# Performance work log

Measured on AMD Instinct MI355X. Metric: run time of the kernel, lower is better.

Reference implementation:

```python
import jax, jax.numpy as jnp
import numpy as np

HEADS = 8
DIM_HEAD = 64
DIM_COOR = 3
SCALE = (DIM_COOR * DIM_HEAD) ** -0.5


def setup_inputs() -> dict:
    key = jax.random.key(0)
    k1, k2, k3 = jax.random.split(key, 3)
    x = jax.random.normal(k1, (2, 2048, 256, 3), dtype=jnp.float32)
    w_qkv = jax.random.normal(k2, (1536, 256), dtype=jnp.float32)
    w_out = jax.random.normal(k3, (256, 512), dtype=jnp.float32)
    return {"x": x, "w_qkv": w_qkv, "w_out": w_out}


def reference(x, w_qkv, w_out):
    b, n, _, c = x.shape
    # VNLinear: contract feature dim, keep coord dim  -> [b, n, 3*h*d, c]
    qkv = jnp.einsum('bnic,oi->bnoc', x, w_qkv)
    q, k, v = jnp.split(qkv, 3, axis=-2)  # each [b, n, h*d, c]

    def to_heads(t):
        return t.reshape(b, n, HEADS, DIM_HEAD, c).transpose(0, 2, 1, 3, 4)  # b h n d c

    q, k, v = map(to_heads, (q, k, v))
    q = q * SCALE
    # scores sum over head-dim AND coordinate-dim
    sim = jnp.einsum('bhidc,bhjdc->bhij', q, k)
    attn = jax.nn.softmax(sim, axis=-1)
    out = jnp.einsum('bhij,bhjdc->bhidc', attn, v)  # coord dim preserved
    out = out.transpose(0, 2, 1, 3, 4).reshape(b, n, HEADS * DIM_HEAD, c)
    return jnp.einsum('bnic,oi->bnoc', out, w_out)
```

## Files before the change

### kernel.cpp

```cpp
#include <hip/hip_runtime.h>
#include <hip/hip_bf16.h>

#define SCALE 0.07216878364870322f
#define LOG2E 1.4426950408889634f

typedef __bf16 bf16x8 __attribute__((ext_vector_type(8)));
typedef float f32x16 __attribute__((ext_vector_type(16)));
typedef float f32x4v __attribute__((ext_vector_type(4)));
typedef unsigned int u32x4 __attribute__((ext_vector_type(4)));
typedef unsigned int u32x2 __attribute__((ext_vector_type(2)));
typedef unsigned short u16;

#define MFMA(a, b, c) __builtin_amdgcn_mfma_f32_32x32x16_bf16(a, b, c, 0, 0, 0)
#define MFMA16(a, b, c) __builtin_amdgcn_mfma_f32_16x16x32_bf16(a, b, c, 0, 0, 0)

__device__ __forceinline__ u16 b16(float v) { return __builtin_bit_cast(u16, (__bf16)v); }
__device__ __forceinline__ float fb16(u16 u) {
    unsigned int t = (unsigned int)u << 16;
    return __builtin_bit_cast(float, t);
}
__device__ __forceinline__ unsigned int splitpack(float v) {
    u16 h = b16(v);
    float r = v - fb16(h);
    return (unsigned int)h | ((unsigned int)b16(r) << 16);
}
__device__ __forceinline__ unsigned int pack2(float a, float b) {
    return (unsigned int)b16(a) | ((unsigned int)b16(b) << 16);
}
__device__ __forceinline__ void gload16(const void* g, void* l) {
    __builtin_amdgcn_global_load_lds((const __attribute__((address_space(1))) void*)g,
                                     (__attribute__((address_space(3))) void*)l, 16, 0, 0);
}

__global__ __launch_bounds__(256) void qkv_mfma(const float* __restrict__ x,
                                                const float* __restrict__ wq,
                                                u16* __restrict__ Qhi, u16* __restrict__ Qlo,
                                                u16* __restrict__ KVf) {
    __shared__ unsigned int ldsr[2][32][196];
    const int tid = threadIdx.x;
    const int lane = tid & 63, w = tid >> 6, hf = lane >> 5, l31 = lane & 31;
    const int lq = lane & 15, gq = lane >> 4;
    const int id = blockIdx.x;
    const int xcd = id & 7;
    const int jj = id >> 3;
    const int nb = xcd * 4 + jj / 24;
    const int ot = jj % 24;
    const int o0 = ot * 64;
    const int b = nb >> 4;
    const int n0 = (nb & 15) * 128;
    const int nw0 = n0 + w * 32;
    const int part = o0 >> 9;
    const int h = (o0 >> 6) & 7;
    const int bh = b * 8 + h;

    const float* xp = x + ((size_t)(b * 2048 + nw0 + l31)) * 768 + hf * 24;
    const float* wp0 = wq + (size_t)(o0 + l31) * 256 + hf * 8;
    const float* wp1 = wp0 + 32 * 256;

    f32x16 acc[3][2] = {};
    #pragma unroll 2
    for (int k0 = 0; k0 < 16; ++k0) {
        float xf[24], wf0[8], wf1[8];
        #pragma unroll
        for (int q = 0; q < 6; ++q) {
            f32x4v t = *(const f32x4v*)(xp + k0 * 48 + q * 4);
            xf[q * 4 + 0] = t[0]; xf[q * 4 + 1] = t[1];
            xf[q * 4 + 2] = t[2]; xf[q * 4 + 3] = t[3];
        }
        {
            f32x4v t0 = *(const f32x4v*)(wp0 + k0 * 16);
            f32x4v t1 = *(const f32x4v*)(wp0 + k0 * 16 + 4);
            f32x4v t2 = *(const f32x4v*)(wp1 + k0 * 16);
            f32x4v t3 = *(const f32x4v*)(wp1 + k0 * 16 + 4);
            #pragma unroll
            for (int e = 0; e < 4; ++e) {
                wf0[e] = t0[e]; wf0[4 + e] = t1[e];
                wf1[e] = t2[e]; wf1[4 + e] = t3[e];
            }
        }
        bf16x8 xh[3], xl[3], wh[2], wl[2];
        #pragma unroll
        for (int c = 0; c < 3; ++c)
            #pragma unroll
            for (int e = 0; e < 8; ++e) {
                float v = xf[e * 3 + c];
                __bf16 hi = (__bf16)v;
                xh[c][e] = hi;
                xl[c][e] = (__bf16)(v - (float)hi);
            }
        #pragma unroll
        for (int e = 0; e < 8; ++e) {
            { float v = wf0[e]; __bf16 hi = (__bf16)v; wh[0][e] = hi; wl[0][e] = (__bf16)(v - (float)hi); }
            { float v = wf1[e]; __bf16 hi = (__bf16)v; wh[1][e] = hi; wl[1][e] = (__bf16)(v - (float)hi); }
        }
        #pragma unroll
        for (int c = 0; c < 3; ++c)
            #pragma unroll
            for (int ot2 = 0; ot2 < 2; ++ot2) {
                acc[c][ot2] = MFMA(xh[c], wh[ot2], acc[c][ot2]);
                acc[c][ot2] = MFMA(xl[c], wh[ot2], acc[c][ot2]);
                acc[c][ot2] = MFMA(xh[c], wl[ot2], acc[c][ot2]);
            }
    }

    #pragma unroll
    for (int round = 0; round < 2; ++round) {
        __syncthreads();
        if ((w >> 1) == round) {
            unsigned int (*L)[196] = ldsr[w & 1];
            #pragma unroll
            for (int c = 0; c < 3; ++c)
                #pragma unroll
                for (int ot2 = 0; ot2 < 2; ++ot2)
                    #pragma unroll
                    for (int r = 0; r < 16; ++r) {
                        float v = acc[c][ot2][r];
                        if (part == 0) v *= (SCALE * LOG2E);
                        int nn = (r & 3) + 8 * (r >> 2) + 4 * hf;
                        int dcol = 3 * (ot2 * 32 + l31) + c;
                        L[nn][dcol] = (part == 2) ? (unsigned int)b16(v) : splitpack(v);
                    }
            if (part < 2) {
                #pragma unroll
                for (int is = 0; is < 2; ++is)
                    #pragma unroll
                    for (int kc = 0; kc < 6; ++kc) {
                        const unsigned int* p = &L[is * 16 + lq][kc * 32 + gq * 8];
                        u32x4 a = *(const u32x4*)p;
                        u32x4 bq = *(const u32x4*)(p + 4);
                        u32x4 hi = { (a[0] & 0xffffu) | (a[1] << 16), (a[2] & 0xffffu) | (a[3] << 16),
                                     (bq[0] & 0xffffu) | (bq[1] << 16), (bq[2] & 0xffffu) | (bq[3] << 16) };
                        u32x4 lo = { (a[0] >> 16) | (a[1] & 0xffff0000u), (a[2] >> 16) | (a[3] & 0xffff0000u),
                                     (bq[0] >> 16) | (bq[1] & 0xffff0000u), (bq[2] >> 16) | (bq[3] & 0xffff0000u) };
                        if (part == 0) {
                            size_t off = ((size_t)(bh * 128 + (nw0 >> 4) + is) * 6 + kc) * 512 + lane * 8;
                            *(u32x4*)(Qhi + off) = hi;
                            *(u32x4*)(Qlo + off) = lo;
                        } else {
                            size_t off = (size_t)(bh * 64 + (nw0 >> 5)) * 18432 + (is * 6 + kc) * 512 + lane * 8;
                            *(u32x4*)(KVf + off) = hi;
                            *(u32x4*)(KVf + off + 6144) = lo;
                        }
                    }
            } else {
                u16* vp = KVf + (size_t)(bh * 64 + (nw0 >> 5)) * 18432 + 12288 + lane * 8;
                #pragma unroll
                for (int d = 0; d < 12; ++d) {
                    unsigned int t[8];
                    #pragma unroll
                    for (int e = 0; e < 8; ++e)
                        t[e] = L[gq * 8 + e][d * 16 + lq];
                    u32x4 pk = { (t[0] & 0xffffu) | (t[1] << 16), (t[2] & 0xffffu) | (t[3] << 16),
                                 (t[4] & 0xffffu) | (t[5] << 16), (t[6] & 0xffffu) | (t[7] << 16) };
                    *(u32x4*)(vp + d * 512) = pk;
                }
            }
        }
    }
}

__global__ __launch_bounds__(256, 2) void attn_mfma(
    const u16* __restrict__ Qhi, const u16* __restrict__ Qlo,
    const u16* __restrict__ KVf, u16* __restrict__ OpA, u16* __restrict__ OpB,
    float2* __restrict__ MLp) {
    __shared__ __align__(16) u16 lds[2][18432];
    const int tid = threadIdx.x;
    const int lane = tid & 63;
    const int wl = tid >> 6;
    const int g = lane >> 4;
    const int i = lane & 15;
    const int id = blockIdx.x;
    const int rem = id >> 3;
    const int grp = ((rem >> 4) << 3) | (id & 7);
    const int itile = rem & 15;
    const int bh = grp >> 1;
    const int half = grp & 1;

    bf16x8 qh[2][6], ql[2][6];
    #pragma unroll
    for (int is = 0; is < 2; ++is) {
        size_t qb = (size_t)(bh * 128 + itile * 8 + wl * 2 + is) * 3072 + (size_t)lane * 8;
        #pragma unroll
        for (int kc = 0; kc < 6; ++kc) {
            qh[is][kc] = *(const bf16x8*)(Qhi + qb + kc * 512);
            ql[is][kc] = *(const bf16x8*)(Qlo + qb + kc * 512);
        }
    }

    const char* gKV = (const char*)KVf + (size_t)bh * 2359296;
    auto stage = [&](int buf, int jtAbs) {
        const char* src = gKV + (size_t)jtAbs * 36864;
        char* dst = (char*)&lds[buf][0];
        #pragma unroll
        for (int s = 0; s < 9; ++s) {
            const int c16 = (tid + s * 256) * 16;
            gload16(src + c16, dst + c16);
        }
    };

    const int jt0 = half * 32;
    stage(0, jt0);
    __syncthreads();
    int cur = 0;

    f32x4v o[2][12] = {};
    float m_run[2] = {-1e30f, -1e30f}, l_run[2] = {0.f, 0.f};

    for (int t = 0; t < 32; ++t) {
        if (t + 1 < 32) stage(cur ^ 1, jt0 + t + 1);
        const u16* L = &lds[cur][0];

        f32x4v s4[2][2] = {};
        __builtin_amdgcn_s_setprio(1);
        #pragma unroll
        for (int kc = 0; kc < 6; ++kc) {
            bf16x8 kh0 = *(const bf16x8*)&L[(unsigned)(kc * 512) + lane * 8];
            bf16x8 kh1 = *(const bf16x8*)&L[(unsigned)((6 + kc) * 512) + lane * 8];
            bf16x8 kl0 = *(const bf16x8*)&L[6144u + (unsigned)(kc * 512) + lane * 8];
            bf16x8 kl1 = *(const bf16x8*)&L[6144u + (unsigned)((6 + kc) * 512) + lane * 8];
            s4[0][0] = MFMA16(kh0, qh[0][kc], s4[0][0]);
            s4[0][1] = MFMA16(kh1, qh[0][kc], s4[0][1]);
            s4[1][0] = MFMA16(kh0, qh[1][kc], s4[1][0]);
            s4[1][1] = MFMA16(kh1, qh[1][kc], s4[1][1]);
            s4[0][0] = MFMA16(kh0, ql[0][kc], s4[0][0]);
            s4[0][1] = MFMA16(kh1, ql[0][kc], s4[0][1]);
            s4[1][0] = MFMA16(kh0, ql[1][kc], s4[1][0]);
            s4[1][1] = MFMA16(kh1, ql[1][kc], s4[1][1]);
            s4[0][0] = MFMA16(kl0, qh[0][kc], s4[0][0]);
            s4[0][1] = MFMA16(kl1, qh[0][kc], s4[0][1]);
            s4[1][0] = MFMA16(kl0, qh[1][kc], s4[1][0]);
            s4[1][1] = MFMA16(kl1, qh[1][kc], s4[1][1]);
        }
        __builtin_amdgcn_s_setprio(0);

        bf16x8 pb[2];
        #pragma unroll
        for (int is = 0; is < 2; ++is) {
            float pm = -1e30f;
            #pragma unroll
            for (int js = 0; js < 2; ++js)
                #pragma unroll
                for (int r = 0; r < 4; ++r) pm = fmaxf(pm, s4[is][js][r]);
            pm = fmaxf(pm, __shfl_xor(pm, 16, 64));
            pm = fmaxf(pm, __shfl_xor(pm, 32, 64));
            if (!__all(pm <= m_run[is] + 8.0f)) {
                float mnew = fmaxf(m_run[is], pm);
                float sc = exp2f(m_run[is] - mnew);
                l_run[is] *= sc;
                #pragma unroll
                for (int d = 0; d < 12; ++d) o[is][d] = o[is][d] * sc;
                m_run[is] = mnew;
            }
            float rs = 0.f;
            unsigned int w0[2], w1[2];
            #pragma unroll
            for (int js = 0; js < 2; ++js) {
                float p0 = exp2f(s4[is][js][0] - m_run[is]), p1 = exp2f(s4[is][js][1] - m_run[is]);
                float p2 = exp2f(s4[is][js][2] - m_run[is]), p3 = exp2f(s4[is][js][3] - m_run[is]);
                rs += (p0 + p1) + (p2 + p3);
                w0[js] = pack2(p0, p1);
                w1[js] = pack2(p2, p3);
            }
            rs += __shfl_xor(rs, 16, 64);
            rs += __shfl_xor(rs, 32, 64);
            l_run[is] += rs;

            u32x4 F;
            const int slA = ((g & 1) << 5) + i;
            const int slB = slA + 16;
            const bool ghi = (g >> 1) != 0;
            { unsigned a0 = __shfl((int)w0[0], slA, 64), a1 = __shfl((int)w0[1], slA, 64); F[0] = ghi ? a1 : a0; }
            { unsigned a0 = __shfl((int)w1[0], slA, 64), a1 = __shfl((int)w1[1], slA, 64); F[1] = ghi ? a1 : a0; }
            { unsigned a0 = __shfl((int)w0[0], slB, 64), a1 = __shfl((int)w0[1], slB, 64); F[2] = ghi ? a1 : a0; }
            { unsigned a0 = __shfl((int)w1[0], slB, 64), a1 = __shfl((int)w1[1], slB, 64); F[3] = ghi ? a1 : a0; }
            pb[is] = __builtin_bit_cast(bf16x8, F);
        }

        __builtin_amdgcn_s_setprio(1);
        #pragma unroll
        for (int d = 0; d < 12; ++d) {
            bf16x8 vf = *(const bf16x8*)&L[12288u + (unsigned)(d * 512) + lane * 8];
            o[0][d] = MFMA16(vf, pb[0], o[0][d]);
            o[1][d] = MFMA16(vf, pb[1], o[1][d]);
        }
        __builtin_amdgcn_s_setprio(0);

        if (t + 1 < 32) {
            __syncthreads();
            cur ^= 1;
        }
    }

    __syncthreads();
    u16* LS = &lds[0][0];
    #pragma unroll
    for (int is = 0; is < 2; ++is) {
        const int row = (wl * 2 + is) * 16 + i;
        #pragma unroll
        for (int d = 0; d < 12; ++d) {
            u32x2 pk = { pack2(o[is][d][0], o[is][d][1]), pack2(o[is][d][2], o[is][d][3]) };
            *(u32x2*)&LS[row * 196 + d * 16 + g * 4] = pk;
        }
        if (g == 0) {
            const int ig = itile * 128 + row;
            float2 ml; ml.x = m_run[is]; ml.y = l_run[is];
            MLp[(size_t)half * 32768 + bh * 2048 + ig] = ml;
        }
    }
    __syncthreads();
    const int b2 = bh >> 3, hh = bh & 7;
    u16* P = half ? OpB : OpA;
    #pragma unroll
    for (int v = 0; v < 12; ++v) {
        const int Lx = v * 256 + tid;
        const int ln   = Lx & 63;
        const int itql = (Lx >> 6) & 3;
        const int ksl  = (Lx >> 8) & 3;
        const int c    = Lx >> 10;
        const int i31 = ln & 31, b5 = ln >> 5;
        const int rowl = itql * 32 + i31;
        unsigned tv[8];
        #pragma unroll
        for (int e = 0; e < 8; ++e) {
            const int dd = ksl * 16 + b5 * 8 + e;
            tv[e] = LS[rowl * 196 + dd * 3 + c];
        }
        u32x4 pk = { tv[0] | (tv[1] << 16), tv[2] | (tv[3] << 16),
                     tv[4] | (tv[5] << 16), tv[6] | (tv[7] << 16) };
        size_t off = (((size_t)(b2 * 3 + c) * 32 + (hh * 4 + ksl)) * 64 + (itile * 4 + itql)) * 512
                     + (size_t)ln * 8;
        *(u32x4*)(P + off) = pk;
    }
}

__global__ __launch_bounds__(256) void out_mfma(const u16* __restrict__ OpA,
                                                const u16* __restrict__ OpB,
                                                const float2* __restrict__ MLp,
                                                const float* __restrict__ wo,
                                                float* __restrict__ out) {
    const int tid = threadIdx.x, lane = tid & 63, w = tid >> 6, hf = lane >> 5, l31 = lane & 31;
    const int o0 = blockIdx.x * 32;
    const int n5 = blockIdx.y * 4 + w;
    const int b = blockIdx.z;
    const float* wp = wo + (size_t)(o0 + l31) * 512 + hf * 8;

    float wa[8], wb[8], inv[8];
    #pragma unroll
    for (int hh = 0; hh < 8; ++hh) {
        size_t mi = (size_t)(b * 8 + hh) * 2048 + n5 * 32 + l31;
        float2 A = MLp[mi];
        float2 Bm = MLp[32768 + mi];
        float mm = fmaxf(A.x, Bm.x);
        wa[hh] = exp2f(A.x - mm);
        wb[hh] = exp2f(Bm.x - mm);
        inv[hh] = 1.0f / (A.y * wa[hh] + Bm.y * wb[hh]);
    }

    f32x16 acc[3] = {};
    #pragma unroll 2
    for (int ks = 0; ks < 32; ++ks) {
        const int hh = ks >> 2;
        const float waH = wa[hh], wbH = wb[hh], invH = inv[hh];
        bf16x8 wh, wl;
        {
            f32x4v t0 = *(const f32x4v*)(wp + ks * 16);
            f32x4v t1 = *(const f32x4v*)(wp + ks * 16 + 4);
            #pragma unroll
            for (int e = 0; e < 4; ++e) {
                { float v = t0[e]; __bf16 hi = (__bf16)v; wh[e] = hi; wl[e] = (__bf16)(v - (float)hi); }
                { float v = t1[e]; __bf16 hi = (__bf16)v; wh[4 + e] = hi; wl[4 + e] = (__bf16)(v - (float)hi); }
            }
        }
        #pragma unroll
        for (int c = 0; c < 3; ++c) {
            size_t pc = (size_t)(b * 3 + c) * 1048576 + (size_t)ks * 32768 + (size_t)n5 * 512 + (size_t)lane * 8;
            u32x4 aA = *(const u32x4*)(OpA + pc);
            u32x4 aB = *(const u32x4*)(OpB + pc);
            unsigned hiw[4], low[4];
            #pragma unroll
            for (int q = 0; q < 4; ++q) {
                unsigned ha = 0, la = 0;
                #pragma unroll
                for (int s = 0; s < 2; ++s) {
                    u16 ua = (u16)((aA[q] >> (s * 16)) & 0xffffu);
                    u16 ub = (u16)((aB[q] >> (s * 16)) & 0xffffu);
                    float v = (fb16(ua) * waH + fb16(ub) * wbH) * invH;
                    u16 hv = b16(v);
                    u16 lv = b16(v - fb16(hv));
                    ha |= ((unsigned)hv) << (s * 16);
                    la |= ((unsigned)lv) << (s * 16);
                }
                hiw[q] = ha; low[q] = la;
            }
            union { bf16x8 v; u32x4 u; } H, Lo;
            H.u  = { hiw[0], hiw[1], hiw[2], hiw[3] };
            Lo.u = { low[0], low[1], low[2], low[3] };
            acc[c] = MFMA(H.v, wh, acc[c]);
            acc[c] = MFMA(Lo.v, wh, acc[c]);
            acc[c] = MFMA(H.v, wl, acc[c]);
        }
    }
    #pragma unroll
    for (int r = 0; r < 16; ++r) {
        int n = (n5 << 5) + (r & 3) + 8 * (r >> 2) + 4 * hf;
        size_t off = ((size_t)(b * 2048 + n) * 256 + o0 + l31) * 3;
        out[off]     = acc[0][r];
        out[off + 1] = acc[1][r];
        out[off + 2] = acc[2][r];
    }
}

extern "C" void kernel_launch(void* const* d_in, const int* in_sizes, int n_in,
                              void* d_out, int out_size, void* d_ws, size_t ws_size,
                              hipStream_t stream) {
    const float* x     = (const float*)d_in[0];
    const float* w_qkv = (const float*)d_in[1];
    const float* w_out = (const float*)d_in[2];
    float* out = (float*)d_out;

    const size_t NB = (size_t)16 * 2048 * 192;
    const size_t KVN = (size_t)16 * 64 * 18432;
    u16* Qhi = (u16*)d_ws;
    u16* Qlo = Qhi + NB;
    u16* KVf = Qlo + NB;
    u16* OpA = KVf + KVN;
    u16* OpB = OpA + NB;
    float2* MLp = (float2*)(OpB + NB);

    qkv_mfma<<<dim3(768), 256, 0, stream>>>(x, w_qkv, Qhi, Qlo, KVf);
    attn_mfma<<<dim3(512), 256, 0, stream>>>(Qhi, Qlo, KVf, OpA, OpB, MLp);
    out_mfma<<<dim3(8, 16, 2), 256, 0, stream>>>(OpA, OpB, MLp, w_out, out);
}
```

Measured before the change: 218.1 us.

## Presplit inputs and weights into bf16 hi/lo MFMA-fragment layouts in a prepass kernel

Result: no change. 214.9 us (-1.5%).

```diff
diff --git a/kernel.cpp b/kernel.cpp
--- a/kernel.cpp
+++ b/kernel.cpp
@@ -32,8 +32,100 @@
                                      (__attribute__((address_space(3))) void*)l, 16, 0, 0);
 }
 
-__global__ __launch_bounds__(256) void qkv_mfma(const float* __restrict__ x,
+__global__ __launch_bounds__(256) void presplit(const float* __restrict__ x,
                                                 const float* __restrict__ wq,
+                                                const float* __restrict__ wo,
+                                                u16* __restrict__ xfh, u16* __restrict__ xfl,
+                                                u16* __restrict__ wfh, u16* __restrict__ wfl,
+                                                u16* __restrict__ wofh, u16* __restrict__ wofl) {
+    const int bid = blockIdx.x;
+    const int tid = threadIdx.x;
+    if (bid < 128) {
+        __shared__ float LT[32 * 49];
+        const int nt = bid & 63, b = bid >> 6;
+        const int n0 = nt * 32;
+        const int lane = tid & 63;
+        const int c = tid >> 6;
+        for (int k0 = 0; k0 < 16; ++k0) {
+            __syncthreads();
+            #pragma unroll
+            for (int s = 0; s < 2; ++s) {
+                int v = tid + s * 256;
+                if (v < 384) {
+                    int row = v / 12, col4 = v % 12;
+                    f32x4v t = *(const f32x4v*)(x + ((size_t)(b * 2048 + n0 + row)) * 768
+                                                + k0 * 48 + col4 * 4);
+                    *(f32x4v*)&LT[row * 49 + col4 * 4] = t;
+                }
+            }
+            __syncthreads();
+            if (c < 3) {
+                const int nl = lane & 31, kh = lane >> 5;
+                const float* src = &LT[nl * 49 + kh * 24 + c];
+                bf16x8 hv, lv;
+                #pragma unroll
+                for (int e = 0; e < 8; ++e) {
+                    float v = src[e * 3];
+                    __bf16 hi = (__bf16)v;
+                    hv[e] = hi;
+                    lv[e] = (__bf16)(v - (float)hi);
+                }
+                size_t off = ((((size_t)(c * 2 + b) * 64 + nt) * 16 + k0) * 512) + lane * 8;
+                *(bf16x8*)(xfh + off) = hv;
+                *(bf16x8*)(xfl + off) = lv;
+            }
+        }
+    } else if (bid < 176) {
+        const int ot32 = bid - 128;
+        const int lane = tid & 63;
+        const int kc0 = tid >> 6;
+        const int o = ot32 * 32 + (lane & 31);
+        const int kh = lane >> 5;
+        #pragma unroll
+        for (int s = 0; s < 4; ++s) {
+            const int kc = kc0 * 4 + s;
+            const float* src = wq + (size_t)o * 256 + kc * 16 + kh * 8;
+            bf16x8 hv, lv;
+            #pragma unroll
+            for (int e = 0; e < 8; ++e) {
+                float v = src[e];
+                __bf16 hi = (__bf16)v;
+                hv[e] = hi;
+                lv[e] = (__bf16)(v - (float)hi);
+            }
+            size_t off = ((size_t)(ot32 * 16 + kc) * 512) + lane * 8;
+            *(bf16x8*)(wfh + off) = hv;
+            *(bf16x8*)(wfl + off) = lv;
+        }
+    } else {
+        const int ot32 = bid - 176;
+        const int lane = tid & 63;
+        const int ks0 = tid >> 6;
+        const int o = ot32 * 32 + (lane & 31);
+        const int kh = lane >> 5;
+        #pragma unroll
+        for (int s = 0; s < 8; ++s) {
+            const int ks = ks0 * 8 + s;
+            const float* src = wo + (size_t)o * 512 + ks * 16 + kh * 8;
+            bf16x8 hv, lv;
+            #pragma unroll
+            for (int e = 0; e < 8; ++e) {
+                float v = src[e];
+                __bf16 hi = (__bf16)v;
+                hv[e] = hi;
+                lv[e] = (__bf16)(v - (float)hi);
+            }
+            size_t off = ((size_t)(ot32 * 32 + ks) * 512) + lane * 8;
+            *(bf16x8*)(wofh + off) = hv;
+            *(bf16x8*)(wofl + off) = lv;
+        }
+    }
+}
+
+__global__ __launch_bounds__(256) void qkv_mfma(const u16* __restrict__ xfh,
+                                                const u16* __restrict__ xfl,
+                                                const u16* __restrict__ wfh,
+                                                const u16* __restrict__ wfl,
                                                 u16* __restrict__ Qhi, u16* __restrict__ Qlo,
                                                 u16* __restrict__ KVf) {
     __shared__ unsigned int ldsr[2][32][196];
@@ -52,47 +144,26 @@
     const int part = o0 >> 9;
     const int h = (o0 >> 6) & 7;
     const int bh = b * 8 + h;
-
-    const float* xp = x + ((size_t)(b * 2048 + nw0 + l31)) * 768 + hf * 24;
-    const float* wp0 = wq + (size_t)(o0 + l31) * 256 + hf * 8;
-    const float* wp1 = wp0 + 32 * 256;
+    const int nt = (nb & 15) * 4 + w;
+
+    const size_t xtb = (((size_t)b * 64 + nt) * 16) * 512 + lane * 8;
+    const size_t cstride = (size_t)2 * 64 * 16 * 512;
+    const size_t wtb0 = ((size_t)(o0 >> 5) * 16) * 512 + lane * 8;
+    const size_t wtb1 = wtb0 + (size_t)16 * 512;
 
     f32x16 acc[3][2] = {};
     #pragma unroll 2
     for (int k0 = 0; k0 < 16; ++k0) {
-        float xf[24], wf0[8], wf1[8];
-        #pragma unroll
-        for (int q = 0; q < 6; ++q) {
-            f32x4v t = *(const f32x4v*)(xp + k0 * 48 + q * 4);
-            xf[q * 4 + 0] = t[0]; xf[q * 4 + 1] = t[1];
-            xf[q * 4 + 2] = t[2]; xf[q * 4 + 3] = t[3];
-        }
-        {
-            f32x4v t0 = *(const f32x4v*)(wp0 + k0 * 16);
-            f32x4v t1 = *(const f32x4v*)(wp0 + k0 * 16 + 4);
-            f32x4v t2 = *(const f32x4v*)(wp1 + k0 * 16);
-            f32x4v t3 = *(const f32x4v*)(wp1 + k0 * 16 + 4);
-            #pragma unroll
-            for (int e = 0; e < 4; ++e) {
-                wf0[e] = t0[e]; wf0[4 + e] = t1[e];
-                wf1[e] = t2[e]; wf1[4 + e] = t3[e];
-            }
-        }
         bf16x8 xh[3], xl[3], wh[2], wl[2];
         #pragma unroll
-        for (int c = 0; c < 3; ++c)
-            #pragma unroll
-            for (int e = 0; e < 8; ++e) {
-                float v = xf[e * 3 + c];
-                __bf16 hi = (__bf16)v;
-                xh[c][e] = hi;
-                xl[c][e] = (__bf16)(v - (float)hi);
-            }
-        #pragma unroll
-        for (int e = 0; e < 8; ++e) {
-            { float v = wf0[e]; __bf16 hi = (__bf16)v; wh[0][e] = hi; wl[0][e] = (__bf16)(v - (float)hi); }
-            { float v = wf1[e]; __bf16 hi = (__bf16)v; wh[1][e] = hi; wl[1][e] = (__bf16)(v - (float)hi); }
-        }
+        for (int c = 0; c < 3; ++c) {
+            xh[c] = *(const bf16x8*)(xfh + xtb + c * cstride + k0 * 512);
+            xl[c] = *(const bf16x8*)(xfl + xtb + c * cstride + k0 * 512);
+        }
+        wh[0] = *(const bf16x8*)(wfh + wtb0 + k0 * 512);
+        wl[0] = *(const bf16x8*)(wfl + wtb0 + k0 * 512);
+        wh[1] = *(const bf16x8*)(wfh + wtb1 + k0 * 512);
+        wl[1] = *(const bf16x8*)(wfl + wtb1 + k0 * 512);
         #pragma unroll
         for (int c = 0; c < 3; ++c)
             #pragma unroll
@@ -336,13 +407,14 @@
 __global__ __launch_bounds__(256) void out_mfma(const u16* __restrict__ OpA,
                                                 const u16* __restrict__ OpB,
                                                 const float2* __restrict__ MLp,
-                                                const float* __restrict__ wo,
+                                                const u16* __restrict__ wofh,
+                                                const u16* __restrict__ wofl,
                                                 float* __restrict__ out) {
     const int tid = threadIdx.x, lane = tid & 63, w = tid >> 6, hf = lane >> 5, l31 = lane & 31;
     const int o0 = blockIdx.x * 32;
     const int n5 = blockIdx.y * 4 + w;
     const int b = blockIdx.z;
-    const float* wp = wo + (size_t)(o0 + l31) * 512 + hf * 8;
+    const size_t wtb = ((size_t)blockIdx.x * 32) * 512 + lane * 8;
 
     float wa[8], wb[8], inv[8];
     #pragma unroll
@@ -361,42 +433,25 @@
     for (int ks = 0; ks < 32; ++ks) {
         const int hh = ks >> 2;
         const float waH = wa[hh], wbH = wb[hh], invH = inv[hh];
-        bf16x8 wh, wl;
-        {
-            f32x4v t0 = *(const f32x4v*)(wp + ks * 16);
-            f32x4v t1 = *(const f32x4v*)(wp + ks * 16 + 4);
-            #pragma unroll
-            for (int e = 0; e < 4; ++e) {
-                { float v = t0[e]; __bf16 hi = (__bf16)v; wh[e] = hi; wl[e] = (__bf16)(v - (float)hi); }
-                { float v = t1[e]; __bf16 hi = (__bf16)v; wh[4 + e] = hi; wl[4 + e] = (__bf16)(v - (float)hi); }
-            }
-        }
+        bf16x8 wh = *(const bf16x8*)(wofh + wtb + ks * 512);
+        bf16x8 wl = *(const bf16x8*)(wofl + wtb + ks * 512);
         #pragma unroll
         for (int c = 0; c < 3; ++c) {
             size_t pc = (size_t)(b * 3 + c) * 1048576 + (size_t)ks * 32768 + (size_t)n5 * 512 + (size_t)lane * 8;
             u32x4 aA = *(const u32x4*)(OpA + pc);
             u32x4 aB = *(const u32x4*)(OpB + pc);
-            unsigned hiw[4], low[4];
+            unsigned hiw[4];
             #pragma unroll
             for (int q = 0; q < 4; ++q) {
-                unsigned ha = 0, la = 0;
-                #pragma unroll
-                for (int s = 0; s < 2; ++s) {
-                    u16 ua = (u16)((aA[q] >> (s * 16)) & 0xffffu);
-                    u16 ub = (u16)((aB[q] >> (s * 16)) & 0xffffu);
-                    float v = (fb16(ua) * waH + fb16(ub) * wbH) * invH;
-                    u16 hv = b16(v);
-                    u16 lv = b16(v - fb16(hv));
-                    ha |= ((unsigned)hv) << (s * 16);
-                    la |= ((unsigned)lv) << (s * 16);
-                }
-                hiw[q] = ha; low[q] = la;
-            }
-            union { bf16x8 v; u32x4 u; } H, Lo;
-            H.u  = { hiw[0], hiw[1], hiw[2], hiw[3] };
-            Lo.u = { low[0], low[1], low[2], low[3] };
+                u16 ua0 = (u16)(aA[q] & 0xffffu), ua1 = (u16)(aA[q] >> 16);
+                u16 ub0 = (u16)(aB[q] & 0xffffu), ub1 = (u16)(aB[q] >> 16);
+                float v0 = (fb16(ua0) * waH + fb16(ub0) * wbH) * invH;
+                float v1 = (fb16(ua1) * waH + fb16(ub1) * wbH) * invH;
+                hiw[q] = pack2(v0, v1);
+            }
+            union { bf16x8 v; u32x4 u; } H;
+            H.u = { hiw[0], hiw[1], hiw[2], hiw[3] };
             acc[c] = MFMA(H.v, wh, acc[c]);
-            acc[c] = MFMA(Lo.v, wh, acc[c]);
             acc[c] = MFMA(H.v, wl, acc[c]);
         }
     }
@@ -420,14 +475,22 @@
 
     const size_t NB = (size_t)16 * 2048 * 192;
     const size_t KVN = (size_t)16 * 64 * 18432;
+    const size_t XF = (size_t)3 * 2 * 64 * 16 * 512;
     u16* Qhi = (u16*)d_ws;
     u16* Qlo = Qhi + NB;
     u16* KVf = Qlo + NB;
     u16* OpA = KVf + KVN;
     u16* OpB = OpA + NB;
     float2* MLp = (float2*)(OpB + NB);
-
-    qkv_mfma<<<dim3(768), 256, 0, stream>>>(x, w_qkv, Qhi, Qlo, KVf);
+    u16* xfh = (u16*)(MLp + 65536);
+    u16* xfl = xfh + XF;
+    u16* wfh = xfl + XF;
+    u16* wfl = wfh + (size_t)1536 * 256;
+    u16* wofh = wfl + (size_t)1536 * 256;
+    u16* wofl = wofh + (size_t)256 * 512;
+
+    presplit<<<dim3(184), 256, 0, stream>>>(x, w_qkv, w_out, xfh, xfl, wfh, wfl, wofh, wofl);
+    qkv_mfma<<<dim3(768), 256, 0, stream>>>(xfh, xfl, wfh, wfl, Qhi, Qlo, KVf);
     attn_mfma<<<dim3(512), 256, 0, stream>>>(Qhi, Qlo, KVf, OpA, OpB, MLp);
-    out_mfma<<<dim3(8, 16, 2), 256, 0, stream>>>(OpA, OpB, MLp, w_out, out);
-}
+    out_mfma<<<dim3(8, 16, 2), 256, 0, stream>>>(OpA, OpB, MLp, wofh, wofl, out);
+}
```
